# Optimization experiments

Measured on AMD Instinct MI355X. Metric: run time of the kernel, lower is better.

Reference implementation:

```python
import jax, jax.numpy as jnp
import numpy as np
from jax.scipy.special import logsumexp

T, NT = 16384, 1024


def setup_inputs() -> dict:
    key = jax.random.key(0)
    k1, k2, k3, k4, k5 = jax.random.split(key, 5)
    return {
        "emit": jax.random.normal(k1, (T, NT), dtype=jnp.float32),
        "y": jax.random.randint(k2, (T,), 0, NT),
        "trans": jax.random.normal(k3, (NT, NT), dtype=jnp.float32),
        "strans": jax.random.normal(k4, (NT,), dtype=jnp.float32),
        "etrans": jax.random.normal(k5, (NT,), dtype=jnp.float32),
    }


def reference(emit, y, trans, strans, etrans):
    # Forward (log-partition) via logsumexp scan over time.
    # torch step: scores = (trans + emit[i]).T; alpha = logsumexp(scores + alpha, dim=1)
    # i.e. alpha_new[k] = emit[i, k] + logsumexp_j(alpha[j] + trans[j, k])
    def step(alpha, e_t):
        alpha_new = e_t + logsumexp(alpha[:, None] + trans, axis=0)
        return alpha_new, None

    alpha0 = strans + emit[0]
    alpha, _ = jax.lax.scan(step, alpha0, emit[1:])
    logZ = logsumexp(alpha + etrans)

    # Gold-path score
    t = emit.shape[0]
    score = (
        strans[y[0]]
        + trans[y[:-1], y[1:]].sum()
        + etrans[y[-1]]
        + emit[jnp.arange(t), y].sum()
    )
    return logZ - score
```

## Files before the change

### kernel.cpp

```cpp
#include <hip/hip_runtime.h>

#define T_LEN 16384
#define NT 1024
#define NBLK 64
#define CPB 16
#define NTHR 256
#define MID 8191

typedef unsigned long long u64;
typedef unsigned int u32;

__device__ __align__(16) u64 g_fbuf[2 * NT];
__device__ __align__(16) u64 g_bbuf[2 * NT];

__device__ __forceinline__ u64 pack_tag(u32 tag, float v) {
  return ((u64)tag << 32) | (u64)__float_as_uint(v);
}
__device__ __forceinline__ u64 ld_tag(const u64* p) {
  return __hip_atomic_load(p, __ATOMIC_RELAXED, __HIP_MEMORY_SCOPE_AGENT);
}
__device__ __forceinline__ void st_tag(u64* p, u64 v) {
  __hip_atomic_store(p, v, __ATOMIC_RELAXED, __HIP_MEMORY_SCOPE_AGENT);
}

__global__ __launch_bounds__(1024) void crf_init(const float* __restrict__ emit,
                                                 const float* __restrict__ strans,
                                                 const float* __restrict__ etrans) {
  int tid = threadIdx.x;
  g_fbuf[tid] = pack_tag(0u, strans[tid] + emit[tid]);
  g_bbuf[tid] = pack_tag(0u, etrans[tid] + emit[(T_LEN - 1) * NT + tid]);
}

__global__ __launch_bounds__(1024) void crf_score(const float* __restrict__ emit,
                                                  const int* __restrict__ y,
                                                  const float* __restrict__ trans,
                                                  const float* __restrict__ strans,
                                                  const float* __restrict__ etrans,
                                                  float* __restrict__ ws) {
  int tid = threadIdx.x;
  float local = 0.f;
  for (int t = tid; t < T_LEN; t += 1024) {
    int yt = y[t];
    local += emit[t * NT + yt];
    if (t > 0) local += trans[y[t - 1] * NT + yt];
  }
  if (tid == 0) local += strans[y[0]];
  if (tid == 1023) local += etrans[y[T_LEN - 1]];
#pragma unroll
  for (int o = 32; o; o >>= 1) local += __shfl_xor(local, o);
  __shared__ float sm[16];
  if ((tid & 63) == 0) sm[tid >> 6] = local;
  __syncthreads();
  if (tid == 0) {
    float s = 0.f;
    for (int i = 0; i < 16; ++i) s += sm[i];
    ws[4096] = s;
  }
}

__global__ __launch_bounds__(NTHR, 1) void crf_scan(const float* __restrict__ emit,
                                                    const float* __restrict__ trans) {
  const int tid = threadIdx.x;
  const bool fwd = blockIdx.x < NBLK;
  const int blk = fwd ? blockIdx.x : (blockIdx.x - NBLK);

  const int c = tid & 15;
  const int chunk = tid >> 4;
  const int col = blk * CPB + c;
  const int wv = tid >> 6;

  u64* buf0 = fwd ? g_fbuf : g_bbuf;
  u64* buf1 = buf0 + NT;
  const int STEPS = fwd ? MID : (T_LEN - 1 - MID);

  float p[64];
  const int jbase = chunk * 64;
#pragma unroll
  for (int i = 0; i < 16; ++i) {
    int off = (4 * i + 8 * chunk) & 63;
#pragma unroll
    for (int x = 0; x < 4; ++x) {
      int jj = jbase + off + x;
      float tv = fwd ? trans[jj * NT + col] : trans[col * NT + jj];
      p[4 * i + x] = __expf(tv);
    }
  }

  __shared__ __align__(16) float aS[NT];
  __shared__ float partS[64];

  float M;
  {
    u64 wd = ld_tag(buf0 + col);
    float v = __uint_as_float((u32)wd);
#pragma unroll
    for (int o = 8; o; o >>= 1) v = fmaxf(v, __shfl_xor(v, o));
    M = v;
  }

  const int i0 = tid, i1 = tid + 256, i2 = tid + 512, i3 = tid + 768;

  for (int n = 1; n <= STEPS; ++n) {
    u64* bIn  = (n & 1) ? buf0 : buf1;
    u64* bOut = (n & 1) ? buf1 : buf0;

    const int te = fwd ? n : (T_LEN - 1 - n);
    float e = emit[te * NT + col];

    const u32 want = (u32)(n - 1);
    u64 w0 = ld_tag(bIn + i0), w1 = ld_tag(bIn + i1);
    u64 w2 = ld_tag(bIn + i2), w3 = ld_tag(bIn + i3);
    for (;;) {
      bool s0 = (u32)(w0 >> 32) != want;
      bool s1 = (u32)(w1 >> 32) != want;
      bool s2 = (u32)(w2 >> 32) != want;
      bool s3 = (u32)(w3 >> 32) != want;
      if (!(s0 | s1 | s2 | s3)) break;
      if (s0) w0 = ld_tag(bIn + i0);
      if (s1) w1 = ld_tag(bIn + i1);
      if (s2) w2 = ld_tag(bIn + i2);
      if (s3) w3 = ld_tag(bIn + i3);
    }
    aS[i0] = __expf(__uint_as_float((u32)w0) - M);
    aS[i1] = __expf(__uint_as_float((u32)w1) - M);
    aS[i2] = __expf(__uint_as_float((u32)w2) - M);
    aS[i3] = __expf(__uint_as_float((u32)w3) - M);
    __syncthreads();

    float s = 0.f;
    const float4* aV = (const float4*)aS;
#pragma unroll
    for (int i = 0; i < 16; ++i) {
      int off = (4 * i + 8 * chunk) & 63;
      float4 a4 = aV[(jbase + off) >> 2];
      s = fmaf(a4.x, p[4 * i + 0], s);
      s = fmaf(a4.y, p[4 * i + 1], s);
      s = fmaf(a4.z, p[4 * i + 2], s);
      s = fmaf(a4.w, p[4 * i + 3], s);
    }
    s += __shfl_xor(s, 16);
    s += __shfl_xor(s, 32);
    if ((tid & 63) < 16) partS[wv * 16 + c] = s;
    __syncthreads();

    float tot = partS[c] + partS[16 + c] + partS[32 + c] + partS[48 + c];
    float anew = e + M + __logf(tot);
    if (tid < 16) st_tag(bOut + col, pack_tag((u32)n, anew));

    float m2 = anew;
#pragma unroll
    for (int o = 8; o; o >>= 1) m2 = fmaxf(m2, __shfl_xor(m2, o));
    M = m2;
  }
}

__global__ __launch_bounds__(1024) void crf_final(const float* __restrict__ emit,
                                                  const float* __restrict__ ws,
                                                  float* __restrict__ out) {
  int tid = threadIdx.x;
  float fa = __uint_as_float((u32)g_fbuf[NT + tid]);
  float bb = __uint_as_float((u32)g_bbuf[tid]);
  float v = fa + bb - emit[MID * NT + tid];
  float m = v;
#pragma unroll
  for (int o = 32; o; o >>= 1) m = fmaxf(m, __shfl_xor(m, o));
  __shared__ float sm[16];
  __shared__ float sM;
  if ((tid & 63) == 0) sm[tid >> 6] = m;
  __syncthreads();
  if (tid == 0) {
    float mm = sm[0];
    for (int i = 1; i < 16; ++i) mm = fmaxf(mm, sm[i]);
    sM = mm;
  }
  __syncthreads();
  float Mv = sM;
  float s = __expf(v - Mv);
#pragma unroll
  for (int o = 32; o; o >>= 1) s += __shfl_xor(s, o);
  __shared__ float ss[16];
  if ((tid & 63) == 0) ss[tid >> 6] = s;
  __syncthreads();
  if (tid == 0) {
    float tot = 0.f;
    for (int i = 0; i < 16; ++i) tot += ss[i];
    float logZ = Mv + __logf(tot);
    out[0] = logZ - ws[4096];
  }
}

extern "C" void kernel_launch(void* const* d_in, const int* in_sizes, int n_in,
                              void* d_out, int out_size, void* d_ws, size_t ws_size,
                              hipStream_t stream) {
  const float* emit = (const float*)d_in[0];
  const int* y = (const int*)d_in[1];
  const float* trans = (const float*)d_in[2];
  const float* strans = (const float*)d_in[3];
  const float* etrans = (const float*)d_in[4];
  float* ws = (float*)d_ws;
  float* out = (float*)d_out;

  crf_init<<<1, 1024, 0, stream>>>(emit, strans, etrans);
  crf_score<<<1, 1024, 0, stream>>>(emit, y, trans, strans, etrans, ws);
  crf_scan<<<2 * NBLK, NTHR, 0, stream>>>(emit, trans);
  crf_final<<<1, 1024, 0, stream>>>(emit, ws, out);
}
```

Measured before the change: 15.18 ms.

## Replace block barriers with per-wave LDS flags and split column ownership across waves

Both __syncthreads calls in the scan loop are replaced with per-wavefront release/acquire flags in shared memory, and each wave now consumes its own contiguous slice of the incoming alpha vector. Each wave finalizes and publishes 4 of the 16 output columns, and the running max is combined from per-wave partial maxima held in double-buffered LDS. The aim is to cut barrier latency on the serial critical path and let waves proceed independently. In exchange it adds spin-polling on LDS flags and more complex cross-wave ordering, relying on workgroup-scope memory semantics for correctness.

```diff
diff --git a/kernel.cpp b/kernel.cpp
--- a/kernel.cpp
+++ b/kernel.cpp
@@ -21,6 +21,12 @@
 }
 __device__ __forceinline__ void st_tag(u64* p, u64 v) {
   __hip_atomic_store(p, v, __ATOMIC_RELAXED, __HIP_MEMORY_SCOPE_AGENT);
+}
+__device__ __forceinline__ int ld_flag(const int* p) {
+  return __hip_atomic_load(p, __ATOMIC_ACQUIRE, __HIP_MEMORY_SCOPE_WORKGROUP);
+}
+__device__ __forceinline__ void st_flag(int* p, int v) {
+  __hip_atomic_store(p, v, __ATOMIC_RELEASE, __HIP_MEMORY_SCOPE_WORKGROUP);
 }
 
 __global__ __launch_bounds__(1024) void crf_init(const float* __restrict__ emit,
@@ -64,52 +70,70 @@
   const bool fwd = blockIdx.x < NBLK;
   const int blk = fwd ? blockIdx.x : (blockIdx.x - NBLK);
 
-  const int c = tid & 15;
-  const int chunk = tid >> 4;
+  const int w = tid >> 6;
+  const int ln = tid & 63;
+  const int c = ln & 15;
+  const int s = ln >> 4;
   const int col = blk * CPB + c;
-  const int wv = tid >> 6;
+  const int colS = blk * CPB + 4 * w + (ln & 3);
 
   u64* buf0 = fwd ? g_fbuf : g_bbuf;
   u64* buf1 = buf0 + NT;
   const int STEPS = fwd ? MID : (T_LEN - 1 - MID);
 
   float p[64];
-  const int jbase = chunk * 64;
+  const int jq = (w << 8) + (s << 6);
 #pragma unroll
   for (int i = 0; i < 16; ++i) {
-    int off = (4 * i + 8 * chunk) & 63;
+    int off = (4 * i + 8 * s) & 63;
 #pragma unroll
     for (int x = 0; x < 4; ++x) {
-      int jj = jbase + off + x;
+      int jj = jq + off + x;
       float tv = fwd ? trans[jj * NT + col] : trans[col * NT + jj];
       p[4 * i + x] = __expf(tv);
     }
   }
 
   __shared__ __align__(16) float aS[NT];
-  __shared__ float partS[64];
-
-  float M;
+  __shared__ float partS[2][4][16];
+  __shared__ float wmax[2][4];
+  __shared__ int flagP[4];
+  __shared__ int flagM[4];
+
+  if (tid < 4) { flagP[tid] = 0; flagM[tid] = 0; }
   {
     u64 wd = ld_tag(buf0 + col);
     float v = __uint_as_float((u32)wd);
 #pragma unroll
     for (int o = 8; o; o >>= 1) v = fmaxf(v, __shfl_xor(v, o));
-    M = v;
-  }
-
-  const int i0 = tid, i1 = tid + 256, i2 = tid + 512, i3 = tid + 768;
+    if (ln == 0) wmax[0][w] = v;
+  }
+  __syncthreads();
+
+  const int i0 = (w << 8) + ln, i1 = i0 + 64, i2 = i0 + 128, i3 = i0 + 192;
 
   for (int n = 1; n <= STEPS; ++n) {
     u64* bIn  = (n & 1) ? buf0 : buf1;
     u64* bOut = (n & 1) ? buf1 : buf0;
+    const int par = n & 1;
 
     const int te = fwd ? n : (T_LEN - 1 - n);
-    float e = emit[te * NT + col];
-
-    const u32 want = (u32)(n - 1);
+
     u64 w0 = ld_tag(bIn + i0), w1 = ld_tag(bIn + i1);
     u64 w2 = ld_tag(bIn + i2), w3 = ld_tag(bIn + i3);
+    float e = emit[te * NT + colS];
+    asm volatile("" ::: "memory");
+
+    for (;;) {
+      int f0 = ld_flag(&flagM[0]), f1 = ld_flag(&flagM[1]);
+      int f2 = ld_flag(&flagM[2]), f3 = ld_flag(&flagM[3]);
+      if (f0 >= n - 1 && f1 >= n - 1 && f2 >= n - 1 && f3 >= n - 1) break;
+    }
+    const int mpar = (n - 1) & 1;
+    float M = fmaxf(fmaxf(wmax[mpar][0], wmax[mpar][1]),
+                    fmaxf(wmax[mpar][2], wmax[mpar][3]));
+
+    const u32 want = (u32)(n - 1);
     for (;;) {
       bool s0 = (u32)(w0 >> 32) != want;
       bool s1 = (u32)(w1 >> 32) != want;
@@ -125,32 +149,39 @@
     aS[i1] = __expf(__uint_as_float((u32)w1) - M);
     aS[i2] = __expf(__uint_as_float((u32)w2) - M);
     aS[i3] = __expf(__uint_as_float((u32)w3) - M);
-    __syncthreads();
-
-    float s = 0.f;
+
+    float sacc = 0.f;
     const float4* aV = (const float4*)aS;
 #pragma unroll
     for (int i = 0; i < 16; ++i) {
-      int off = (4 * i + 8 * chunk) & 63;
-      float4 a4 = aV[(jbase + off) >> 2];
-      s = fmaf(a4.x, p[4 * i + 0], s);
-      s = fmaf(a4.y, p[4 * i + 1], s);
-      s = fmaf(a4.z, p[4 * i + 2], s);
-      s = fmaf(a4.w, p[4 * i + 3], s);
-    }
-    s += __shfl_xor(s, 16);
-    s += __shfl_xor(s, 32);
-    if ((tid & 63) < 16) partS[wv * 16 + c] = s;
-    __syncthreads();
-
-    float tot = partS[c] + partS[16 + c] + partS[32 + c] + partS[48 + c];
+      int off = (4 * i + 8 * s) & 63;
+      float4 a4 = aV[(jq + off) >> 2];
+      sacc = fmaf(a4.x, p[4 * i + 0], sacc);
+      sacc = fmaf(a4.y, p[4 * i + 1], sacc);
+      sacc = fmaf(a4.z, p[4 * i + 2], sacc);
+      sacc = fmaf(a4.w, p[4 * i + 3], sacc);
+    }
+    sacc += __shfl_xor(sacc, 16);
+    sacc += __shfl_xor(sacc, 32);
+    if (ln < 16) partS[par][w][c] = sacc;
+    st_flag(&flagP[w], n);
+
+    for (;;) {
+      int f0 = ld_flag(&flagP[0]), f1 = ld_flag(&flagP[1]);
+      int f2 = ld_flag(&flagP[2]), f3 = ld_flag(&flagP[3]);
+      if (f0 >= n && f1 >= n && f2 >= n && f3 >= n) break;
+    }
+    const int cs = 4 * w + (ln & 3);
+    float tot = partS[par][0][cs] + partS[par][1][cs] +
+                partS[par][2][cs] + partS[par][3][cs];
     float anew = e + M + __logf(tot);
-    if (tid < 16) st_tag(bOut + col, pack_tag((u32)n, anew));
+    if (ln < 4) st_tag(bOut + colS, pack_tag((u32)n, anew));
 
     float m2 = anew;
-#pragma unroll
-    for (int o = 8; o; o >>= 1) m2 = fmaxf(m2, __shfl_xor(m2, o));
-    M = m2;
+    m2 = fmaxf(m2, __shfl_xor(m2, 1));
+    m2 = fmaxf(m2, __shfl_xor(m2, 2));
+    if (ln == 0) wmax[par][w] = m2;
+    st_flag(&flagM[w], n);
   }
 }
 
```

Result: slower. 18.32 ms (+20.7%).
